# Kernel tuning notes

Measured on AMD Instinct MI355X. Metric: run time of the kernel, lower is better.

## Reference

```python
import jax, jax.numpy as jnp
import numpy as np

EPS = 1e-12  # torch F.normalize clamp_min eps


def _agnn_conv(x, src, dst, beta, n):
    # x: [N, D]; src/dst: [E] (message flows src -> dst, softmax over dst's in-edges)
    xn = x / jnp.maximum(jnp.linalg.norm(x, axis=-1, keepdims=True), EPS)
    alpha = beta[0] * jnp.sum(xn[src] * xn[dst], axis=-1)            # [E] cosine sim * beta
    amax = jax.ops.segment_max(alpha, dst, num_segments=n)           # stable segment softmax
    ex = jnp.exp(alpha - amax[dst])
    denom = jax.ops.segment_sum(ex, dst, num_segments=n)
    w = ex / denom[dst]                                              # [E]
    return jax.ops.segment_sum(x[src] * w[:, None], dst, num_segments=n)


def setup_inputs() -> dict:
    key = jax.random.key(0)
    ks = jax.random.split(key, 8)
    N, E, G = 131072, 4194304, 2048
    x = jax.random.normal(ks[0], (N, 75), dtype=jnp.float32)
    edge_index = jax.random.randint(ks[1], (2, E), 0, N, dtype=jnp.int64)
    batch = jnp.sort(jax.random.randint(ks[2], (N,), 0, G, dtype=jnp.int64))
    lin1_w = jax.random.normal(ks[3], (16, 75), dtype=jnp.float32) * (1.0 / np.sqrt(75))
    lin1_b = jnp.zeros((16,), jnp.float32)
    beta1 = jnp.ones((1,), jnp.float32)   # prop1: requires_grad=False, beta=1
    beta2 = jnp.ones((1,), jnp.float32)   # prop2: learnable beta, init 1
    lin2_w = jax.random.normal(ks[4], (64, 16), dtype=jnp.float32) * (1.0 / np.sqrt(16))
    lin2_b = jnp.zeros((64,), jnp.float32)
    gather_w = jax.random.normal(ks[5], (1, 64), dtype=jnp.float32) * (1.0 / np.sqrt(64))
    gather_b = jnp.zeros((1,), jnp.float32)
    return {"x": x, "edge_index": edge_index, "batch": batch, "num_graphs": G,
            "lin1_w": lin1_w, "lin1_b": lin1_b, "beta1": beta1, "beta2": beta2,
            "lin2_w": lin2_w, "lin2_b": lin2_b, "gather_w": gather_w, "gather_b": gather_b}


def reference(x, edge_index, batch, num_graphs, lin1_w, lin1_b, beta1, beta2,
              lin2_w, lin2_b, gather_w, gather_b):
    n = x.shape[0]
    # PyG AGNNConv adds self-loops by default
    loops = jnp.arange(n, dtype=edge_index.dtype)
    src = jnp.concatenate([edge_index[0], loops])
    dst = jnp.concatenate([edge_index[1], loops])
    # dropout is identity in eval mode
    h = jax.nn.relu(x @ lin1_w.T + lin1_b)          # [N, 16]
    h = _agnn_conv(h, src, dst, beta1, n)
    h = _agnn_conv(h, src, dst, beta2, n)
    h = h @ lin2_w.T + lin2_b                        # [N, 64]
    y = jax.ops.segment_sum(h, batch, num_segments=num_graphs)  # global_add_pool [G, 64]
    return y @ gather_w.T + gather_b                 # [G, 1]
```

## Files before the change

kernel.cpp:

```cpp
#include <hip/hip_runtime.h>
#include <hip/hip_bf16.h>
#include <hip/hip_fp16.h>
#include <math.h>

#define SSEPS 1e-24f
#define NPB 256
#define NPB_SHIFT 8
#define SRC_BITS 17
#define SRC_MASK ((1 << SRC_BITS) - 1)
#define NB 512
#define CAP_B 8832
#define SC_EDGES 4096
#define SCB 512
#define MG_T 512
#define MG_SCAT 1024
#define MG_LIN 4096
#define CSR_T 512

union QRowU2 { int4 v; _Float16 h[8]; };


__global__ __launch_bounds__(MG_T) void mega1(
    const int* __restrict__ src, const int* __restrict__ dst, int E,
    int* __restrict__ gcursor, int* __restrict__ packed,
    const float* __restrict__ x, const float* __restrict__ W1,
    const float* __restrict__ b1, int* __restrict__ rec1, int N, int D,
    const float* __restrict__ l2w, const float* __restrict__ l2b,
    const float* __restrict__ gw, float* __restrict__ vbuf,
    float* __restrict__ out, const float* __restrict__ gb, int G) {
    __shared__ int sh[2 * SC_EDGES + 3 * SCB];
    int bid = blockIdx.x;
    int t = threadIdx.x;

    if (bid < MG_SCAT) {
        int* lout = sh;
        int* loutd = sh + SC_EDGES;
        int* h = sh + 2 * SC_EDGES;
        int* s = h + SCB;
        int* delta = s + SCB;
        int base = bid * SC_EDGES;
        int cnt = E - base;
        if (cnt > SC_EDGES) cnt = SC_EDGES;

        h[t] = 0;
        __syncthreads();
        for (int i = t; i < cnt; i += MG_T)
            atomicAdd(&h[dst[base + i] >> NPB_SHIFT], 1);
        __syncthreads();
        s[t] = h[t];
        __syncthreads();
        for (int off = 1; off < SCB; off <<= 1) {
            int a = (t >= off) ? s[t - off] : 0;
            __syncthreads();
            s[t] += a;
            __syncthreads();
        }
        {
            int c = h[t];
            int ex = s[t] - c;
            int gp = c ? atomicAdd(&gcursor[t], c) : 0;
            delta[t] = (t * CAP_B + gp) - ex;
            h[t] = ex;
        }
        __syncthreads();
        for (int i = t; i < cnt; i += MG_T) {
            int d = dst[base + i];
            int b = d >> NPB_SHIFT;
            int pos = atomicAdd(&h[b], 1);
            lout[pos] = ((d & (NPB - 1)) << SRC_BITS) | src[base + i];
            loutd[pos] = delta[b] + pos;
        }
        __syncthreads();
        for (int i = t; i < cnt; i += MG_T)
            packed[loutd[i]] = lout[i];
    } else if (bid < MG_SCAT + MG_LIN) {
        float* Ws = (float*)sh;
        float* Bs = Ws + 16 * 75;
        for (int i = t; i < 16 * D; i += MG_T) Ws[i] = W1[i];
        if (t < 16) Bs[t] = b1[t];
        __syncthreads();
        int node = (bid - MG_SCAT) * (MG_T >> 4) + (t >> 4);
        int c = t & 15;
        if (node >= N) return;
        const float* xr = x + (size_t)node * D;
        float acc = Bs[c];
        for (int k = 0; k < D; ++k) acc = fmaf(xr[k], Ws[c * D + k], acc);
        float hv = fmaxf(acc, 0.f);
        float hn = __shfl_xor(hv, 1);
        if (!(c & 1)) {
            union { _Float16 hh[2]; int i; } u;
            u.hh[0] = (_Float16)hv;
            u.hh[1] = (_Float16)hn;
            rec1[8 * node + (c >> 1)] = u.i;
        }
    } else if (bid == MG_SCAT + MG_LIN) {
        if (t < 16) {
            float a = 0.f;
            for (int j = 0; j < 64; ++j) a = fmaf(gw[j], l2w[j * 16 + t], a);
            vbuf[t] = a;
        } else if (t == 16) {
            float a = 0.f;
            for (int j = 0; j < 64; ++j) a = fmaf(gw[j], l2b[j], a);
            vbuf[16] = a;
        }
    } else {
        int g = (bid - (MG_SCAT + MG_LIN + 1)) * MG_T + t;
        if (g < G) out[g] = gb[0];
    }
}

__global__ __launch_bounds__(CSR_T) void csr_build(
    const int* __restrict__ packed, const int* __restrict__ gcursor,
    int* __restrict__ deg, int* __restrict__ offs,
    int* __restrict__ csr_src, int N) {
    __shared__ int lout[CAP_B];
    __shared__ int ldeg[NPB];
    __shared__ int lofs[NPB];
    int b = blockIdx.x;
    int t = threadIdx.x;
    int e0 = b * CAP_B;
    int cnt = gcursor[b];
    if (t < NPB) ldeg[t] = 0;
    __syncthreads();
    for (int i = t; i < cnt; i += CSR_T)
        atomicAdd(&ldeg[packed[e0 + i] >> SRC_BITS], 1);
    __syncthreads();
    int v = (t < NPB) ? ldeg[t] : 0;
    if (t < NPB) lofs[t] = v;
    __syncthreads();
    for (int off = 1; off < NPB; off <<= 1) {
        int u = (t < NPB && t >= off) ? lofs[t - off] : 0;
        __syncthreads();
        if (t < NPB) lofs[t] += u;
        __syncthreads();
    }
    if (t < NPB) {
        int ex = lofs[t] - v;
        int node = (b << NPB_SHIFT) + t;
        if (node < N) {
            deg[node] = v;
            offs[node] = e0 + ex;
        }
        lofs[t] = ex;
    }
    __syncthreads();
    for (int i = t; i < cnt; i += CSR_T) {
        int p = packed[e0 + i];
        int pos = atomicAdd(&lofs[p >> SRC_BITS], 1);
        lout[pos] = p & SRC_MASK;
    }
    __syncthreads();
    for (int i = t; i < cnt; i += CSR_T)
        csr_src[e0 + i] = lout[i];
}

__global__ __launch_bounds__(256) void agnn_conv1(
    const int* __restrict__ rec1,
    const int* __restrict__ offs, const int* __restrict__ deg,
    const int* __restrict__ csr, const float* __restrict__ beta_p,
    int* __restrict__ rec2, int N) {
    int tid = blockIdx.x * blockDim.x + threadIdx.x;
    int node = tid >> 1;
    int q = tid & 1;
    if (node >= N) return;
    float beta = beta_p[0];
    const int4* rp = (const int4*)rec1;

    QRowU2 rdu;
    rdu.v = rp[2 * node + q];
    float xd[8];
#pragma unroll
    for (int k = 0; k < 8; ++k) xd[k] = (float)rdu.h[k];

    float ssd = 0.f;
#pragma unroll
    for (int k = 0; k < 8; ++k) ssd = fmaf(xd[k], xd[k], ssd);
    ssd += __shfl_xor(ssd, 1);
    float invsd = rsqrtf(fmaxf(ssd, SSEPS));

    float e0 = __expf(beta * ssd * invsd * invsd);
    float denom = e0;
    float acc[8];
#pragma unroll
    for (int k = 0; k < 8; ++k) acc[k] = e0 * xd[k];

    int start = offs[node], cnt = deg[node];
    int i = 0;
    for (; i + 8 <= cnt; i += 8) {
        int j[8];
        QRowU2 r[8];
#pragma unroll
        for (int u = 0; u < 8; ++u) j[u] = __builtin_nontemporal_load(&csr[start + i + u]);
#pragma unroll
        for (int u = 0; u < 8; ++u) r[u].v = rp[2 * j[u] + q];
#pragma unroll
        for (int u = 0; u < 8; ++u) {
            float d = 0.f, ss = 0.f;
            float hs[8];
#pragma unroll
            for (int k = 0; k < 8; ++k) {
                hs[k] = (float)r[u].h[k];
                d = fmaf(xd[k], hs[k], d);
                ss = fmaf(hs[k], hs[k], ss);
            }
            d += __shfl_xor(d, 1);
            ss += __shfl_xor(ss, 1);
            float ee = __expf(beta * d * invsd * rsqrtf(fmaxf(ss, SSEPS)));
            denom += ee;
#pragma unroll
            for (int k = 0; k < 8; ++k) acc[k] = fmaf(ee, hs[k], acc[k]);
        }
    }
    for (; i < cnt; ++i) {
        int j = __builtin_nontemporal_load(&csr[start + i]);
        QRowU2 r;
        r.v = rp[2 * j + q];
        float d = 0.f, ss = 0.f;
        float hs[8];
#pragma unroll
        for (int k = 0; k < 8; ++k) {
            hs[k] = (float)r.h[k];
            d = fmaf(xd[k], hs[k], d);
            ss = fmaf(hs[k], hs[k], ss);
        }
        d += __shfl_xor(d, 1);
        ss += __shfl_xor(ss, 1);
        float ee = __expf(beta * d * invsd * rsqrtf(fmaxf(ss, SSEPS)));
        denom += ee;
#pragma unroll
        for (int k = 0; k < 8; ++k) acc[k] = fmaf(ee, hs[k], acc[k]);
    }

    float inv = 1.f / denom;
    QRowU2 w;
#pragma unroll
    for (int k = 0; k < 8; ++k) w.h[k] = (_Float16)(acc[k] * inv);
    ((int4*)rec2)[2 * node + q] = w.v;
}

__global__ __launch_bounds__(256) void agnn_conv2(
    const int* __restrict__ rec2,
    const int* __restrict__ offs, const int* __restrict__ deg,
    const int* __restrict__ csr, const float* __restrict__ beta_p,
    const float* __restrict__ vbuf,
    float* __restrict__ rbuf, int N) {
    int tid = blockIdx.x * blockDim.x + threadIdx.x;
    int node = tid >> 1;
    int q = tid & 1;
    if (node >= N) return;
    float beta = beta_p[0];
    const int4* rp = (const int4*)rec2;

    float vq[8];
#pragma unroll
    for (int k = 0; k < 8; ++k) vq[k] = vbuf[8 * q + k];

    QRowU2 rdu;
    rdu.v = rp[2 * node + q];
    float xd[8];
#pragma unroll
    for (int k = 0; k < 8; ++k) xd[k] = (float)rdu.h[k];

    float ssd = 0.f, pd = 0.f;
#pragma unroll
    for (int k = 0; k < 8; ++k) {
        ssd = fmaf(xd[k], xd[k], ssd);
        pd = fmaf(vq[k], xd[k], pd);
    }
    ssd += __shfl_xor(ssd, 1);
    pd += __shfl_xor(pd, 1);
    float invsd = rsqrtf(fmaxf(ssd, SSEPS));

    float e0 = __expf(beta * ssd * invsd * invsd);
    float denom = e0;
    float acc = e0 * pd;

    int start = offs[node], cnt = deg[node];
    int i = 0;
    for (; i + 8 <= cnt; i += 8) {
        int j[8];
        QRowU2 r[8];
#pragma unroll
        for (int u = 0; u < 8; ++u) j[u] = __builtin_nontemporal_load(&csr[start + i + u]);
#pragma unroll
        for (int u = 0; u < 8; ++u) r[u].v = rp[2 * j[u] + q];
#pragma unroll
        for (int u = 0; u < 8; ++u) {
            float d = 0.f, ss = 0.f, pv = 0.f;
#pragma unroll
            for (int k = 0; k < 8; ++k) {
                float hs = (float)r[u].h[k];
                d = fmaf(xd[k], hs, d);
                ss = fmaf(hs, hs, ss);
                pv = fmaf(vq[k], hs, pv);
            }
            d += __shfl_xor(d, 1);
            ss += __shfl_xor(ss, 1);
            pv += __shfl_xor(pv, 1);
            float ee = __expf(beta * d * invsd * rsqrtf(fmaxf(ss, SSEPS)));
            denom += ee;
            acc = fmaf(ee, pv, acc);
        }
    }
    for (; i < cnt; ++i) {
        int j = __builtin_nontemporal_load(&csr[start + i]);
        QRowU2 r;
        r.v = rp[2 * j + q];
        float d = 0.f, ss = 0.f, pv = 0.f;
#pragma unroll
        for (int k = 0; k < 8; ++k) {
            float hs = (float)r.h[k];
            d = fmaf(xd[k], hs, d);
            ss = fmaf(hs, hs, ss);
            pv = fmaf(vq[k], hs, pv);
        }
        d += __shfl_xor(d, 1);
        ss += __shfl_xor(ss, 1);
        pv += __shfl_xor(pv, 1);
        float ee = __expf(beta * d * invsd * rsqrtf(fmaxf(ss, SSEPS)));
        denom += ee;
        acc = fmaf(ee, pv, acc);
    }
    if (q == 0) rbuf[node] = acc / denom;
}

__global__ void pool_kernel(const float* __restrict__ r, const int* __restrict__ batch,
                            const float* __restrict__ vbuf, float* __restrict__ out,
                            int N) {
    int base = (blockIdx.x * blockDim.x + threadIdx.x) * 8;
    if (base >= N) return;
    float c0 = vbuf[16];
    int lim = base + 8;
    if (lim > N) lim = N;
    float run = 0.f;
    int g = -1;
    for (int i = base; i < lim; ++i) {
        int gi = batch[i];
        if (gi != g) {
            if (g >= 0) atomicAdd(&out[g], run);
            g = gi;
            run = 0.f;
        }
        run += r[i] + c0;
    }
    if (g >= 0) atomicAdd(&out[g], run);
}


extern "C" void kernel_launch(void* const* d_in, const int* in_sizes, int n_in,
                              void* d_out, int out_size, void* d_ws, size_t ws_size,
                              hipStream_t stream) {
    const float* x = (const float*)d_in[0];
    const int* edge_index = (const int*)d_in[1];
    const int* batch = (const int*)d_in[2];
    const float* lin1_w = (const float*)d_in[4];
    const float* lin1_b = (const float*)d_in[5];
    const float* beta1 = (const float*)d_in[6];
    const float* beta2 = (const float*)d_in[7];
    const float* lin2_w = (const float*)d_in[8];
    const float* lin2_b = (const float*)d_in[9];
    const float* gather_w = (const float*)d_in[10];
    const float* gather_b = (const float*)d_in[11];
    float* out = (float*)d_out;

    const int N = in_sizes[2];
    const int E = in_sizes[1] / 2;
    const int D = in_sizes[0] / N;
    const int G = out_size;

    const int* src = edge_index;
    const int* dst = edge_index + E;

    float* w = (float*)d_ws;
    int* rec1 = (int*)w;                 w += (size_t)N * 8;
    int* rec2 = (int*)w;                 w += (size_t)N * 8;
    float* rbuf = w;                     w += N;
    float* vbuf = w;                     w += 32;
    int* deg = (int*)w;                  w += N;
    int* offs = (int*)w;                 w += N;
    int* packed = (int*)w;               w += (size_t)NB * CAP_B;
    int* csr_src = (int*)w;              w += (size_t)NB * CAP_B;
    int* gcursor = (int*)w;              w += NB;

    const int B = 256;
    dim3 gridNode2((2 * N + B - 1) / B);

    hipMemsetAsync(gcursor, 0, NB * sizeof(int), stream);

    int nScat = (E + SC_EDGES - 1) / SC_EDGES;
    int nLin = (N + (MG_T / 16) - 1) / (MG_T / 16);
    int nOut = (G + MG_T - 1) / MG_T;
    dim3 megaGrid(nScat + nLin + 1 + nOut);
    mega1<<<megaGrid, MG_T, 0, stream>>>(src, dst, E, gcursor, packed,
                                         x, lin1_w, lin1_b, rec1, N, D,
                                         lin2_w, lin2_b, gather_w, vbuf,
                                         out, gather_b, G);

    csr_build<<<dim3(NB), CSR_T, 0, stream>>>(packed, gcursor, deg, offs,
                                              csr_src, N);

    agnn_conv1<<<gridNode2, B, 0, stream>>>(rec1, offs, deg, csr_src,
                                            beta1, rec2, N);
    agnn_conv2<<<gridNode2, B, 0, stream>>>(rec2, offs, deg, csr_src,
                                            beta2, vbuf, rbuf, N);

    pool_kernel<<<dim3((N / 8 + B - 1) / B), B, 0, stream>>>(rbuf, batch, vbuf, out, N);
}
```

Measured before the change: 282.2 us.

## Drop LDS staging in bucket scatter and CSR build, fuse pooling into conv2

The edge-bucketing phase now keeps each thread's edges in registers and writes packed entries straight to global memory. This removes the in-block prefix scan and the LDS staging arrays, so LDS use drops sharply and more blocks can be resident. csr_build swaps its barrier-heavy scan for a wavefront shuffle scan and scatters directly to csr_src instead of staging through LDS. The separate pool kernel is removed: conv2 atomically adds each node's result into its graph's output, which raises contention on the global atomics. Writes become less coalesced, and a capacity guard now drops edges that overflow a bucket.

```diff
diff --git a/kernel.cpp b/kernel.cpp
--- a/kernel.cpp
+++ b/kernel.cpp
@@ -13,7 +13,6 @@
 #define SC_EDGES 4096
 #define SCB 512
 #define MG_T 512
-#define MG_SCAT 1024
 #define MG_LIN 4096
 #define CSR_T 512
 
@@ -22,64 +21,57 @@
 
 __global__ __launch_bounds__(MG_T) void mega1(
     const int* __restrict__ src, const int* __restrict__ dst, int E,
-    int* __restrict__ gcursor, int* __restrict__ packed,
+    int* __restrict__ gcnt, int* __restrict__ packed, int nScat,
     const float* __restrict__ x, const float* __restrict__ W1,
     const float* __restrict__ b1, int* __restrict__ rec1, int N, int D,
     const float* __restrict__ l2w, const float* __restrict__ l2b,
     const float* __restrict__ gw, float* __restrict__ vbuf,
     float* __restrict__ out, const float* __restrict__ gb, int G) {
-    __shared__ int sh[2 * SC_EDGES + 3 * SCB];
+    __shared__ int sh[1216];
     int bid = blockIdx.x;
     int t = threadIdx.x;
 
-    if (bid < MG_SCAT) {
-        int* lout = sh;
-        int* loutd = sh + SC_EDGES;
-        int* h = sh + 2 * SC_EDGES;
-        int* s = h + SCB;
-        int* delta = s + SCB;
+    if (bid < nScat) {
+        int* h = sh;
+        int* dl = sh + SCB;
         int base = bid * SC_EDGES;
-        int cnt = E - base;
-        if (cnt > SC_EDGES) cnt = SC_EDGES;
-
+        int ed[8], es[8];
+        int nv = 0;
+#pragma unroll
+        for (int k = 0; k < 8; ++k) {
+            int i = base + k * MG_T + t;
+            if (i < E) {
+                ed[nv] = __builtin_nontemporal_load(&dst[i]);
+                es[nv] = __builtin_nontemporal_load(&src[i]);
+                ++nv;
+            }
+        }
         h[t] = 0;
         __syncthreads();
-        for (int i = t; i < cnt; i += MG_T)
-            atomicAdd(&h[dst[base + i] >> NPB_SHIFT], 1);
+        for (int k = 0; k < nv; ++k) atomicAdd(&h[ed[k] >> NPB_SHIFT], 1);
         __syncthreads();
-        s[t] = h[t];
-        __syncthreads();
-        for (int off = 1; off < SCB; off <<= 1) {
-            int a = (t >= off) ? s[t - off] : 0;
-            __syncthreads();
-            s[t] += a;
-            __syncthreads();
-        }
         {
             int c = h[t];
-            int ex = s[t] - c;
-            int gp = c ? atomicAdd(&gcursor[t], c) : 0;
-            delta[t] = (t * CAP_B + gp) - ex;
-            h[t] = ex;
+            int gp = c ? atomicAdd(&gcnt[t], c) : 0;
+            dl[t] = t * CAP_B + gp;
+            h[t] = 0;
         }
         __syncthreads();
-        for (int i = t; i < cnt; i += MG_T) {
-            int d = dst[base + i];
+        for (int k = 0; k < nv; ++k) {
+            int d = ed[k];
             int b = d >> NPB_SHIFT;
             int pos = atomicAdd(&h[b], 1);
-            lout[pos] = ((d & (NPB - 1)) << SRC_BITS) | src[base + i];
-            loutd[pos] = delta[b] + pos;
-        }
-        __syncthreads();
-        for (int i = t; i < cnt; i += MG_T)
-            packed[loutd[i]] = lout[i];
-    } else if (bid < MG_SCAT + MG_LIN) {
+            int gi = dl[b] + pos;
+            if (gi < (b + 1) * CAP_B)
+                packed[gi] = ((d & (NPB - 1)) << SRC_BITS) | es[k];
+        }
+    } else if (bid < nScat + MG_LIN) {
         float* Ws = (float*)sh;
-        float* Bs = Ws + 16 * 75;
+        float* Bs = (float*)sh + 1200;
         for (int i = t; i < 16 * D; i += MG_T) Ws[i] = W1[i];
         if (t < 16) Bs[t] = b1[t];
         __syncthreads();
-        int node = (bid - MG_SCAT) * (MG_T >> 4) + (t >> 4);
+        int node = (bid - nScat) * (MG_T >> 4) + (t >> 4);
         int c = t & 15;
         if (node >= N) return;
         const float* xr = x + (size_t)node * D;
@@ -93,7 +85,7 @@
             u.hh[1] = (_Float16)hn;
             rec1[8 * node + (c >> 1)] = u.i;
         }
-    } else if (bid == MG_SCAT + MG_LIN) {
+    } else if (bid == nScat + MG_LIN) {
         if (t < 16) {
             float a = 0.f;
             for (int j = 0; j < 64; ++j) a = fmaf(gw[j], l2w[j * 16 + t], a);
@@ -104,54 +96,59 @@
             vbuf[16] = a;
         }
     } else {
-        int g = (bid - (MG_SCAT + MG_LIN + 1)) * MG_T + t;
+        int g = (bid - (nScat + MG_LIN + 1)) * MG_T + t;
         if (g < G) out[g] = gb[0];
     }
 }
 
 __global__ __launch_bounds__(CSR_T) void csr_build(
-    const int* __restrict__ packed, const int* __restrict__ gcursor,
+    const int* __restrict__ packed, const int* __restrict__ gcnt,
     int* __restrict__ deg, int* __restrict__ offs,
     int* __restrict__ csr_src, int N) {
-    __shared__ int lout[CAP_B];
     __shared__ int ldeg[NPB];
-    __shared__ int lofs[NPB];
+    __shared__ int lcur[NPB];
+    __shared__ int wsum[4];
     int b = blockIdx.x;
     int t = threadIdx.x;
     int e0 = b * CAP_B;
-    int cnt = gcursor[b];
+    int cnt = gcnt[b];
+    if (cnt > CAP_B) cnt = CAP_B;
     if (t < NPB) ldeg[t] = 0;
     __syncthreads();
     for (int i = t; i < cnt; i += CSR_T)
         atomicAdd(&ldeg[packed[e0 + i] >> SRC_BITS], 1);
     __syncthreads();
-    int v = (t < NPB) ? ldeg[t] : 0;
-    if (t < NPB) lofs[t] = v;
+    if (t < NPB) {
+        int v = ldeg[t];
+        int lane = t & 63;
+        int incl = v;
+#pragma unroll
+        for (int off = 1; off < 64; off <<= 1) {
+            int up = __shfl_up(incl, off);
+            if (lane >= off) incl += up;
+        }
+        if (lane == 63) wsum[t >> 6] = incl;
+        lcur[t] = incl - v;
+    }
     __syncthreads();
-    for (int off = 1; off < NPB; off <<= 1) {
-        int u = (t < NPB && t >= off) ? lofs[t - off] : 0;
-        __syncthreads();
-        if (t < NPB) lofs[t] += u;
-        __syncthreads();
-    }
     if (t < NPB) {
-        int ex = lofs[t] - v;
+        int w = t >> 6;
+        int basep = 0;
+        for (int k = 0; k < w; ++k) basep += wsum[k];
+        int ex = lcur[t] + basep;
         int node = (b << NPB_SHIFT) + t;
         if (node < N) {
-            deg[node] = v;
+            deg[node] = ldeg[t];
             offs[node] = e0 + ex;
         }
-        lofs[t] = ex;
+        lcur[t] = ex;
     }
     __syncthreads();
     for (int i = t; i < cnt; i += CSR_T) {
         int p = packed[e0 + i];
-        int pos = atomicAdd(&lofs[p >> SRC_BITS], 1);
-        lout[pos] = p & SRC_MASK;
-    }
-    __syncthreads();
-    for (int i = t; i < cnt; i += CSR_T)
-        csr_src[e0 + i] = lout[i];
+        int pos = atomicAdd(&lcur[p >> SRC_BITS], 1);
+        csr_src[e0 + pos] = p & SRC_MASK;
+    }
 }
 
 __global__ __launch_bounds__(256) void agnn_conv1(
@@ -242,8 +239,8 @@
     const int* __restrict__ rec2,
     const int* __restrict__ offs, const int* __restrict__ deg,
     const int* __restrict__ csr, const float* __restrict__ beta_p,
-    const float* __restrict__ vbuf,
-    float* __restrict__ rbuf, int N) {
+    const float* __restrict__ vbuf, const int* __restrict__ batch,
+    float* __restrict__ out, int N) {
     int tid = blockIdx.x * blockDim.x + threadIdx.x;
     int node = tid >> 1;
     int q = tid & 1;
@@ -321,29 +318,7 @@
         denom += ee;
         acc = fmaf(ee, pv, acc);
     }
-    if (q == 0) rbuf[node] = acc / denom;
-}
-
-__global__ void pool_kernel(const float* __restrict__ r, const int* __restrict__ batch,
-                            const float* __restrict__ vbuf, float* __restrict__ out,
-                            int N) {
-    int base = (blockIdx.x * blockDim.x + threadIdx.x) * 8;
-    if (base >= N) return;
-    float c0 = vbuf[16];
-    int lim = base + 8;
-    if (lim > N) lim = N;
-    float run = 0.f;
-    int g = -1;
-    for (int i = base; i < lim; ++i) {
-        int gi = batch[i];
-        if (gi != g) {
-            if (g >= 0) atomicAdd(&out[g], run);
-            g = gi;
-            run = 0.f;
-        }
-        run += r[i] + c0;
-    }
-    if (g >= 0) atomicAdd(&out[g], run);
+    if (q == 0) atomicAdd(&out[batch[node]], acc / denom + vbuf[16]);
 }
 
 
@@ -374,35 +349,32 @@
     float* w = (float*)d_ws;
     int* rec1 = (int*)w;                 w += (size_t)N * 8;
     int* rec2 = (int*)w;                 w += (size_t)N * 8;
-    float* rbuf = w;                     w += N;
     float* vbuf = w;                     w += 32;
     int* deg = (int*)w;                  w += N;
     int* offs = (int*)w;                 w += N;
     int* packed = (int*)w;               w += (size_t)NB * CAP_B;
     int* csr_src = (int*)w;              w += (size_t)NB * CAP_B;
-    int* gcursor = (int*)w;              w += NB;
+    int* gcnt = (int*)w;                 w += NB;
 
     const int B = 256;
     dim3 gridNode2((2 * N + B - 1) / B);
 
-    hipMemsetAsync(gcursor, 0, NB * sizeof(int), stream);
+    hipMemsetAsync(gcnt, 0, NB * sizeof(int), stream);
 
     int nScat = (E + SC_EDGES - 1) / SC_EDGES;
     int nLin = (N + (MG_T / 16) - 1) / (MG_T / 16);
     int nOut = (G + MG_T - 1) / MG_T;
     dim3 megaGrid(nScat + nLin + 1 + nOut);
-    mega1<<<megaGrid, MG_T, 0, stream>>>(src, dst, E, gcursor, packed,
+    mega1<<<megaGrid, MG_T, 0, stream>>>(src, dst, E, gcnt, packed, nScat,
                                          x, lin1_w, lin1_b, rec1, N, D,
                                          lin2_w, lin2_b, gather_w, vbuf,
                                          out, gather_b, G);
 
-    csr_build<<<dim3(NB), CSR_T, 0, stream>>>(packed, gcursor, deg, offs,
+    csr_build<<<dim3(NB), CSR_T, 0, stream>>>(packed, gcnt, deg, offs,
                                               csr_src, N);
 
     agnn_conv1<<<gridNode2, B, 0, stream>>>(rec1, offs, deg, csr_src,
                                             beta1, rec2, N);
     agnn_conv2<<<gridNode2, B, 0, stream>>>(rec2, offs, deg, csr_src,
-                                            beta2, vbuf, rbuf, N);
-
-    pool_kernel<<<dim3((N / 8 + B - 1) / B), B, 0, stream>>>(rbuf, batch, vbuf, out, N);
-}
+                                            beta2, vbuf, batch, out, N);
+}
```

New measurement: 332.7 us. 1.18x slower.
